# Optimization experiments

Measured on AMD Instinct MI355X. Metric: run time of the kernel, lower is better.

Reference implementation:

```python
import jax, jax.numpy as jnp
import numpy as np

N, C, H, W = 8, 4, 256, 256
SMOOTH = 1e-6


def _edt_to_zeros(m):
    """Exact Euclidean distance transform of a 2D mask [H, W]:
    distance from each pixel to the nearest pixel where m == 0
    (matches scipy.ndimage.distance_transform_edt(m)).
    Separable algorithm: 1D row distances, then min over rows of g^2 + di^2.
    """
    Hh, Ww = m.shape
    BIG = jnp.float32(Hh + Ww)  # larger than any achievable 1D distance
    z = m == 0
    j = jnp.arange(Ww, dtype=jnp.float32)
    # nearest zero to the left / right within each row
    left = jax.lax.cummax(jnp.where(z, j, -BIG), axis=1)
    right = jax.lax.cummin(jnp.where(z, j, 2.0 * BIG), axis=1, reverse=True)
    g = jnp.minimum(jnp.minimum(j - left, right - j), BIG)  # [H, W]
    i = jnp.arange(Hh, dtype=jnp.float32)
    di2 = (i[:, None] - i[None, :]) ** 2  # [H(i), H(k)]
    # d2[i, j] = min_k g[k, j]^2 + (i - k)^2 ; [H, H, W] broadcast, min over k
    d2 = jnp.min(g[None, :, :] ** 2 + di2[:, :, None], axis=1)
    return jnp.sqrt(d2)


def _signed_edt(m):
    # scipy: dt_pos = edt(mask) (dist to nearest zero), dt_neg = edt(1 - mask)
    return _edt_to_zeros(m) - _edt_to_zeros(1.0 - m)


def setup_inputs() -> dict:
    key = jax.random.key(0)
    k1, k2 = jax.random.split(key)
    input_tensor = jax.random.normal(k1, (N, C, H, W), dtype=jnp.float32)
    target = jax.random.randint(k2, (N, H, W), 0, C, dtype=jnp.int32)
    return {"input_tensor": input_tensor, "target": target}


def reference(input_tensor, target):
    probs = jax.nn.softmax(input_tensor, axis=1)            # [N, C, H, W]
    onehot = jax.nn.one_hot(target, C, dtype=jnp.float32)   # [N, H, W, C]
    masks = jnp.moveaxis(onehot, -1, 0).reshape(C * N, H, W)
    # one EDT at a time to bound the [H, H, W] intermediate
    sdt = jax.lax.map(_signed_edt, masks).reshape(C, N, H, W)
    bl = jnp.einsum('nchw,cnhw->cn', probs, sdt)            # per-class, per-sample sums
    # torch: sum_c mean_n(bl / (H*W + smooth)) / C == mean_{c,n}(bl) / (H*W + smooth)
    return jnp.mean(bl) / (H * W + SMOOTH)
```

## Files before the change

kernel.cpp:

```cpp
#include <hip/hip_runtime.h>

#define Nn 8
#define Cc 4
#define Hh 256
#define Ww 256

typedef unsigned int u32;
typedef unsigned short u16;
typedef u16 u16x4 __attribute__((ext_vector_type(4)));
typedef unsigned long long u64;

#define OFF_PART 0

__global__ __launch_bounds__(1024) void merged_kernel(
    const int* __restrict__ tgt, const float* __restrict__ in,
    float* __restrict__ partials) {
  __shared__ u16x4 s2[32][64];
  __shared__ float s_w[16];
  const int bid = blockIdx.x;
  const int n = bid >> 6;
  const int it = (bid >> 2) & 15;
  const int jt = bid & 3;
  const int i0 = it * 16, j0 = jt * 64;
  const int tid = threadIdx.x;
  const int lane = tid & 63;
  const int w = tid >> 6;
  const int j = j0 + lane;
  const int i = i0 + w;

  const long cs = (long)Hh * Ww;
  const float* lp = in + ((long)(n * Cc) * Hh + i) * Ww + j;
  const float x0 = lp[0];
  const float x1 = lp[cs];
  const float x2 = lp[2 * cs];
  const float x3 = lp[3 * cs];

  const int k0r = i0 - 8 + 2 * w;
  int t_[2][4];
#pragma unroll
  for (int rr = 0; rr < 2; ++rr) {
    const int kc = min(max(k0r + rr, 0), Hh - 1);
    const int rowOff = (n * Hh + kc) * Ww + lane;
#pragma unroll
    for (int q = 0; q < 4; ++q) t_[rr][q] = tgt[rowOff + q * 64];
  }

  const int lane16 = lane + 16;
  const bool c0 = (lane16 < 32);
  const bool c1 = (lane16 >= 32) && (lane16 < 64);
  const u32 shift = (u32)(lane16 & 31);
  const u16 SENT = 0xFE00;

#pragma unroll
  for (int rr = 0; rr < 2; ++rr) {
    const int r = 2 * w + rr;
    const int k = k0r + rr;
    u16x4 sq = {SENT, SENT, SENT, SENT};
    if (k >= 0 && k < Hh) {
      u16 dv[4];
#pragma unroll
      for (int c = 0; c < Cc; ++c) {
        const u64 M0 = __ballot(t_[rr][0] == c);
        const u64 M1 = __ballot(t_[rr][1] == c);
        const u64 M2 = __ballot(t_[rr][2] == c);
        const u64 M3 = __ballot(t_[rr][3] == c);
        const u32 W0 = (u32)M0, W1 = (u32)(M0 >> 32);
        const u32 W2 = (u32)M1, W3 = (u32)(M1 >> 32);
        const u32 W4 = (u32)M2, W5 = (u32)(M2 >> 32);
        const u32 W6 = (u32)M3, W7 = (u32)(M3 >> 32);
        const u32 U0 = (jt == 0) ? 0u : ((jt == 1) ? W1 : ((jt == 2) ? W3 : W5));
        const u32 U1 = (jt == 0) ? W0 : ((jt == 1) ? W2 : ((jt == 2) ? W4 : W6));
        const u32 U2 = (jt == 0) ? W1 : ((jt == 1) ? W3 : ((jt == 2) ? W5 : W7));
        const u32 U3 = (jt == 0) ? W2 : ((jt == 1) ? W4 : ((jt == 2) ? W6 : 0u));
        const u32 lo = c0 ? U0 : (c1 ? U1 : U2);
        const u32 hi = c0 ? U1 : (c1 ? U2 : U3);
        const u32 win = __builtin_amdgcn_alignbit(hi, lo, shift);
        const u32 ml = win & 0x1FFFFu;
        const u32 mr = win >> 16;
        const int dl = __builtin_clz(ml | 1u) - 15;
        const int dr = __builtin_ctz(mr | 0x10000u);
        const int dd = min(min(dl, dr), 10);
        dv[c] = (u16)(dd * dd);
      }
      sq.x = dv[0]; sq.y = dv[1]; sq.z = dv[2]; sq.w = dv[3];
    }
    s2[r][lane] = sq;
  }
  __syncthreads();

  u16x4 acc = s2[w + 8][lane];
#pragma unroll
  for (int o = 1; o <= 8; ++o) {
    const u16x4 pr =
        __builtin_elementwise_min(s2[w + 8 - o][lane], s2[w + 8 + o][lane]);
    const u16 dd = (u16)(o * o);
    const u16x4 ddv = {dd, dd, dd, dd};
    acc = __builtin_elementwise_min(acc, pr + ddv);
  }
  int d0 = acc.x, d1 = acc.y, d2 = acc.z, d3 = acc.w;

  if (max(max(d0, d1), max(d2, d3)) > 81) {
    d0 = 0x7fffffff; d1 = 0x7fffffff; d2 = 0x7fffffff; d3 = 0x7fffffff;
    const int* tp = tgt + n * (Hh * Ww);
    for (int p = 0; p < Hh * Ww; ++p) {
      const int t = tp[p];
      const int dy = i - (p >> 8);
      const int dx = j - (p & 255);
      const int dd2 = dy * dy + dx * dx;
      d0 = (t == 0) ? min(d0, dd2) : d0;
      d1 = (t == 1) ? min(d1, dd2) : d1;
      d2 = (t == 2) ? min(d2, dd2) : d2;
      d3 = (t == 3) ? min(d3, dd2) : d3;
    }
  }

  const float f0 = (float)d0, f1 = (float)d1;
  const float f2 = (float)d2, f3 = (float)d3;
  const float mx = fmaxf(fmaxf(x0, x1), fmaxf(x2, x3));
  const float e0 = __expf(x0 - mx), e1 = __expf(x1 - mx);
  const float e2 = __expf(x2 - mx), e3 = __expf(x3 - mx);
  const float rs = __builtin_amdgcn_rcpf(e0 + e1 + e2 + e3);
  const float p0 = e0 * rs, p1 = e1 * rs, p2 = e2 * rs, p3 = e3 * rs;
  const int q0 = (d0 == 0) ? 0x7fffffff : d0;
  const int q1 = (d1 == 0) ? 0x7fffffff : d1;
  const int q2 = (d2 == 0) ? 0x7fffffff : d2;
  const int q3 = (d3 == 0) ? 0x7fffffff : d3;
  const float dbar = (float)min(min(q0, q1), min(q2, q3));
  const float pt = (d0 == 0) ? p0 : (d1 == 0) ? p1 : (d2 == 0) ? p2 : p3;
  float contrib = pt * __builtin_amdgcn_sqrtf(dbar) -
                  (p0 * __builtin_amdgcn_sqrtf(f0) +
                   p1 * __builtin_amdgcn_sqrtf(f1) +
                   p2 * __builtin_amdgcn_sqrtf(f2) +
                   p3 * __builtin_amdgcn_sqrtf(f3));

#pragma unroll
  for (int off = 32; off > 0; off >>= 1) contrib += __shfl_down(contrib, off);
  if (lane == 0) s_w[w] = contrib;
  __syncthreads();
  if (tid == 0) {
    float v = 0.0f;
#pragma unroll
    for (int q = 0; q < 16; ++q) v += s_w[q];
    partials[bid] = v;
  }
}

__global__ __launch_bounds__(256) void finalize_kernel(
    const float* __restrict__ partials, float* __restrict__ out) {
  __shared__ float s_red[256];
  const int tid = threadIdx.x;
  const float v0 = partials[tid];
  const float v1 = partials[tid + 256];
  s_red[tid] = v0 + v1;
  __syncthreads();
  for (int st = 128; st > 0; st >>= 1) {
    if (tid < st) s_red[tid] += s_red[tid + st];
    __syncthreads();
  }
  if (tid == 0)
    out[0] = s_red[0] / (float)(Cc * Nn) / (65536.0f + 1e-6f);
}

extern "C" void kernel_launch(void* const* d_in, const int* in_sizes, int n_in,
                              void* d_out, int out_size, void* d_ws, size_t ws_size,
                              hipStream_t stream) {
  const float* input = (const float*)d_in[0];
  const int* target = (const int*)d_in[1];
  float* out = (float*)d_out;
  float* partials = (float*)((char*)d_ws + OFF_PART);

  merged_kernel<<<dim3(512), dim3(1024), 0, stream>>>(target, input, partials);
  finalize_kernel<<<dim3(1), dim3(256), 0, stream>>>(partials, out);
}
```

Baseline: 14.00 us.

## Replace finalize kernel with last-block atomic reduction and load only neighbor target tiles

Removes the separate finalize kernel launch. Each block instead quantizes its partial sum to fixed-point and atomically adds it into a 64-bit accumulator, and the last block to arrive, detected through an atomic counter, writes the final result. A memset zeroes the accumulator and counter before launch. Separately, each thread now loads three target column tiles (left neighbor, own, right neighbor) instead of all four, which cuts global loads and ballots per class. The fixed-point quantization adds a small rounding error. The release/acquire ordering between the accumulator add and the counter add relies on device atomics.

```diff
diff --git a/kernel.cpp b/kernel.cpp
--- a/kernel.cpp
+++ b/kernel.cpp
@@ -10,11 +10,10 @@
 typedef u16 u16x4 __attribute__((ext_vector_type(4)));
 typedef unsigned long long u64;
 
-#define OFF_PART 0
 
 __global__ __launch_bounds__(1024) void merged_kernel(
     const int* __restrict__ tgt, const float* __restrict__ in,
-    float* __restrict__ partials) {
+    u64* __restrict__ acc, u32* __restrict__ cnt, float* __restrict__ out) {
   __shared__ u16x4 s2[32][64];
   __shared__ float s_w[16];
   const int bid = blockIdx.x;
@@ -36,13 +35,16 @@
   const float x3 = lp[3 * cs];
 
   const int k0r = i0 - 8 + 2 * w;
-  int t_[2][4];
+  const int cm1 = (jt == 0) ? 0 : (jt - 1);
+  const int cp1 = (jt == 3) ? 3 : (jt + 1);
+  int t_[2][3];
 #pragma unroll
   for (int rr = 0; rr < 2; ++rr) {
     const int kc = min(max(k0r + rr, 0), Hh - 1);
     const int rowOff = (n * Hh + kc) * Ww + lane;
-#pragma unroll
-    for (int q = 0; q < 4; ++q) t_[rr][q] = tgt[rowOff + q * 64];
+    t_[rr][0] = tgt[rowOff + cm1 * 64];
+    t_[rr][1] = tgt[rowOff + jt * 64];
+    t_[rr][2] = tgt[rowOff + cp1 * 64];
   }
 
   const int lane16 = lane + 16;
@@ -60,18 +62,13 @@
       u16 dv[4];
 #pragma unroll
       for (int c = 0; c < Cc; ++c) {
-        const u64 M0 = __ballot(t_[rr][0] == c);
-        const u64 M1 = __ballot(t_[rr][1] == c);
-        const u64 M2 = __ballot(t_[rr][2] == c);
-        const u64 M3 = __ballot(t_[rr][3] == c);
-        const u32 W0 = (u32)M0, W1 = (u32)(M0 >> 32);
-        const u32 W2 = (u32)M1, W3 = (u32)(M1 >> 32);
-        const u32 W4 = (u32)M2, W5 = (u32)(M2 >> 32);
-        const u32 W6 = (u32)M3, W7 = (u32)(M3 >> 32);
-        const u32 U0 = (jt == 0) ? 0u : ((jt == 1) ? W1 : ((jt == 2) ? W3 : W5));
-        const u32 U1 = (jt == 0) ? W0 : ((jt == 1) ? W2 : ((jt == 2) ? W4 : W6));
-        const u32 U2 = (jt == 0) ? W1 : ((jt == 1) ? W3 : ((jt == 2) ? W5 : W7));
-        const u32 U3 = (jt == 0) ? W2 : ((jt == 1) ? W4 : ((jt == 2) ? W6 : 0u));
+        const u64 Bm1 = __ballot(t_[rr][0] == c);
+        const u64 B0  = __ballot(t_[rr][1] == c);
+        const u64 Bp1 = __ballot(t_[rr][2] == c);
+        const u32 U0 = (jt == 0) ? 0u : (u32)(Bm1 >> 32);
+        const u32 U1 = (u32)B0;
+        const u32 U2 = (u32)(B0 >> 32);
+        const u32 U3 = (jt == 3) ? 0u : (u32)Bp1;
         const u32 lo = c0 ? U0 : (c1 ? U1 : U2);
         const u32 hi = c0 ? U1 : (c1 ? U2 : U3);
         const u32 win = __builtin_amdgcn_alignbit(hi, lo, shift);
@@ -88,16 +85,16 @@
   }
   __syncthreads();
 
-  u16x4 acc = s2[w + 8][lane];
+  u16x4 acc4 = s2[w + 8][lane];
 #pragma unroll
   for (int o = 1; o <= 8; ++o) {
     const u16x4 pr =
         __builtin_elementwise_min(s2[w + 8 - o][lane], s2[w + 8 + o][lane]);
     const u16 dd = (u16)(o * o);
     const u16x4 ddv = {dd, dd, dd, dd};
-    acc = __builtin_elementwise_min(acc, pr + ddv);
+    acc4 = __builtin_elementwise_min(acc4, pr + ddv);
   }
-  int d0 = acc.x, d1 = acc.y, d2 = acc.z, d3 = acc.w;
+  int d0 = acc4.x, d1 = acc4.y, d2 = acc4.z, d3 = acc4.w;
 
   if (max(max(d0, d1), max(d2, d3)) > 81) {
     d0 = 0x7fffffff; d1 = 0x7fffffff; d2 = 0x7fffffff; d3 = 0x7fffffff;
@@ -141,24 +138,16 @@
     float v = 0.0f;
 #pragma unroll
     for (int q = 0; q < 16; ++q) v += s_w[q];
-    partials[bid] = v;
+    const long long qi = (long long)llrintf(v * 1048576.0f);
+    const u64 oldacc = atomicAdd(acc, (u64)qi);
+    asm volatile("" ::"v"(oldacc));
+    const u32 oldc = atomicAdd(cnt, 1u);
+    if (oldc == 511u) {
+      const u64 tot = atomicAdd(acc, 0ull);
+      const double sum = (double)(long long)tot * (1.0 / 1048576.0);
+      out[0] = (float)(sum / (double)(Cc * Nn) / (65536.0 + 1e-6));
+    }
   }
-}
-
-__global__ __launch_bounds__(256) void finalize_kernel(
-    const float* __restrict__ partials, float* __restrict__ out) {
-  __shared__ float s_red[256];
-  const int tid = threadIdx.x;
-  const float v0 = partials[tid];
-  const float v1 = partials[tid + 256];
-  s_red[tid] = v0 + v1;
-  __syncthreads();
-  for (int st = 128; st > 0; st >>= 1) {
-    if (tid < st) s_red[tid] += s_red[tid + st];
-    __syncthreads();
-  }
-  if (tid == 0)
-    out[0] = s_red[0] / (float)(Cc * Nn) / (65536.0f + 1e-6f);
 }
 
 extern "C" void kernel_launch(void* const* d_in, const int* in_sizes, int n_in,
@@ -167,8 +156,10 @@
   const float* input = (const float*)d_in[0];
   const int* target = (const int*)d_in[1];
   float* out = (float*)d_out;
-  float* partials = (float*)((char*)d_ws + OFF_PART);
+  u64* acc = (u64*)d_ws;
+  u32* cnt = (u32*)((char*)d_ws + 8);
 
-  merged_kernel<<<dim3(512), dim3(1024), 0, stream>>>(target, input, partials);
-  finalize_kernel<<<dim3(1), dim3(256), 0, stream>>>(partials, out);
+  hipMemsetAsync(d_ws, 0, 16, stream);
+  merged_kernel<<<dim3(512), dim3(1024), 0, stream>>>(target, input, acc, cnt,
+                                                      out);
 }
```

New measurement: 26.13 us. +86.7%, slower.
